# Kernel optimization log

Measured on AMD Instinct MI355X. Metric: run time of the kernel, lower is better.

The kernel has to match this reference:

```python
import jax, jax.numpy as jnp
import numpy as np

N, C, H, W = 64, 256, 56, 56
SIZE = 51          # odd number of spline knots per activation
GRID = 0.1         # knot spacing


def setup_inputs() -> dict:
    key = jax.random.key(0)
    x = jax.random.normal(key, (N, C, H, W), dtype=jnp.float32)

    # Coefficient init identical to the module: first half of channels use |grid|,
    # second half use softshrink(grid, lambd=0.5).
    half_knots = SIZE // 2
    grid_arange = jnp.arange(-half_knots, half_knots + 1, dtype=jnp.float32) * GRID  # [SIZE]
    grid_tensor = jnp.broadcast_to(grid_arange, (C, SIZE))                           # [C, SIZE]
    halfC = C // 2
    softshrunk = jnp.where(grid_tensor > 0.5, grid_tensor - 0.5,
                           jnp.where(grid_tensor < -0.5, grid_tensor + 0.5, 0.0))
    coeffs = jnp.concatenate([jnp.abs(grid_tensor[:halfC]), softshrunk[halfC:]], axis=0)
    coefficients_vect = coeffs.reshape(-1)                                           # [C*SIZE]

    zero_knot_indexes = jnp.arange(C, dtype=jnp.int32) * SIZE + half_knots           # [C]
    return {"x": x, "coefficients_vect": coefficients_vect,
            "zero_knot_indexes": zero_knot_indexes}


def reference(x, coefficients_vect, zero_knot_indexes):
    half_knots = SIZE // 2
    # Clamp so that idx and idx+1 stay inside this activation's knot range.
    x_clamped = jnp.clip(x, -GRID * half_knots, GRID * (half_knots - 1))
    floored = jnp.floor(x_clamped / GRID)               # left knot offset (float)
    fracs = x / GRID - floored                          # fractional position (uses unclamped x)
    idx = zero_knot_indexes[None, :, None, None] + floored.astype(jnp.int32)  # [N,C,H,W]
    c0 = coefficients_vect[idx]
    c1 = coefficients_vect[idx + 1]
    return c1 * fracs + c0 * (1.0 - fracs)
```

## Files before the change

### kernel.cpp

```cpp
#include <hip/hip_runtime.h>


typedef float f32x4 __attribute__((ext_vector_type(4)));

constexpr int C_CH  = 256;
constexpr int KSIZE = 51;
constexpr int HW    = 56 * 56;
constexpr int HW4   = HW / 4;

__device__ __forceinline__ f32x4 bspline4(f32x4 v, const float2* sc, int bias) {
    f32x4 r;
    #pragma unroll
    for (int k = 0; k < 4; ++k) {
        float xe = v[k];
        float xc = fminf(fmaxf(xe, -2.5f), 2.4f);
        float fl = floorf(xc * 10.0f);
        float fr = xe * 10.0f - fl;
        float2 cc = sc[(int)fl + bias];
        r[k] = cc.y * fr + cc.x * (1.0f - fr);
    }
    return r;
}

__global__ __launch_bounds__(256)
void bspline_act_kernel(const float* __restrict__ x,
                        const float* __restrict__ coeff,
                        const int*   __restrict__ zk,
                        float*       __restrict__ out)
{
    const int p   = blockIdx.x;
    const int c   = p & (C_CH - 1);
    const int tid = threadIdx.x;

    __shared__ float2 sc[KSIZE - 1];
    if (tid < KSIZE - 1) {
        float a = coeff[c * KSIZE + tid];
        float b = coeff[c * KSIZE + tid + 1];
        sc[tid] = make_float2(a, b);
    }
    const int bias = zk[c] - c * KSIZE;
    __syncthreads();

    const f32x4* __restrict__ xv = (const f32x4*)(x + (size_t)p * HW);
    f32x4*       __restrict__ ov = (f32x4*)(out + (size_t)p * HW);

    f32x4 v0 = __builtin_nontemporal_load(&xv[tid]);
    f32x4 v1 = __builtin_nontemporal_load(&xv[tid + 256]);
    f32x4 v2 = __builtin_nontemporal_load(&xv[tid + 512]);
    const bool tail = tid < (HW4 - 768);
    f32x4 v3;
    if (tail) v3 = __builtin_nontemporal_load(&xv[tid + 768]);

    f32x4 r0 = bspline4(v0, sc, bias);
    f32x4 r1 = bspline4(v1, sc, bias);
    f32x4 r2 = bspline4(v2, sc, bias);
    __builtin_nontemporal_store(r0, &ov[tid]);
    __builtin_nontemporal_store(r1, &ov[tid + 256]);
    __builtin_nontemporal_store(r2, &ov[tid + 512]);
    if (tail) {
        f32x4 r3 = bspline4(v3, sc, bias);
        __builtin_nontemporal_store(r3, &ov[tid + 768]);
    }
}

extern "C" void kernel_launch(void* const* d_in, const int* in_sizes, int n_in,
                              void* d_out, int out_size, void* d_ws, size_t ws_size,
                              hipStream_t stream) {
    const float* x     = (const float*)d_in[0];
    const float* coeff = (const float*)d_in[1];
    const int*   zk    = (const int*)d_in[2];
    float*       out   = (float*)d_out;

    const int n_planes = out_size / HW;
    bspline_act_kernel<<<n_planes, 256, 0, stream>>>(x, coeff, zk, out);
}
```

Measured before the change: 68.87 us.

## Process eight batch planes per block with register double-buffered loads

```diff
diff --git a/kernel.cpp b/kernel.cpp
--- a/kernel.cpp
+++ b/kernel.cpp
@@ -7,6 +7,7 @@
 constexpr int KSIZE = 51;
 constexpr int HW    = 56 * 56;
 constexpr int HW4   = HW / 4;
+constexpr int PPB   = 8;
 
 __device__ __forceinline__ f32x4 bspline4(f32x4 v, const float2* sc, int bias) {
     f32x4 r;
@@ -28,38 +29,53 @@
                         const int*   __restrict__ zk,
                         float*       __restrict__ out)
 {
-    const int p   = blockIdx.x;
-    const int c   = p & (C_CH - 1);
+    const int bid = blockIdx.x;
+    const int c   = bid & (C_CH - 1);
+    const int n0  = (bid >> 8) * PPB;
     const int tid = threadIdx.x;
+
+    const size_t  base    = ((size_t)n0 * C_CH + c) * HW;
+    const size_t  vstride = (size_t)C_CH * HW / 4;
+    const f32x4* __restrict__ xv = (const f32x4*)(x + base);
+    f32x4*       __restrict__ ov = (f32x4*)(out + base);
+
+    const bool tail = tid < (HW4 - 768);
+
+    f32x4 a0 = __builtin_nontemporal_load(xv + tid);
+    f32x4 a1 = __builtin_nontemporal_load(xv + tid + 256);
+    f32x4 a2 = __builtin_nontemporal_load(xv + tid + 512);
+    f32x4 a3 = {0,0,0,0};
+    if (tail) a3 = __builtin_nontemporal_load(xv + tid + 768);
 
     __shared__ float2 sc[KSIZE - 1];
     if (tid < KSIZE - 1) {
-        float a = coeff[c * KSIZE + tid];
-        float b = coeff[c * KSIZE + tid + 1];
-        sc[tid] = make_float2(a, b);
+        float va = coeff[c * KSIZE + tid];
+        float vb = coeff[c * KSIZE + tid + 1];
+        sc[tid] = make_float2(va, vb);
     }
     const int bias = zk[c] - c * KSIZE;
     __syncthreads();
 
-    const f32x4* __restrict__ xv = (const f32x4*)(x + (size_t)p * HW);
-    f32x4*       __restrict__ ov = (f32x4*)(out + (size_t)p * HW);
-
-    f32x4 v0 = __builtin_nontemporal_load(&xv[tid]);
-    f32x4 v1 = __builtin_nontemporal_load(&xv[tid + 256]);
-    f32x4 v2 = __builtin_nontemporal_load(&xv[tid + 512]);
-    const bool tail = tid < (HW4 - 768);
-    f32x4 v3;
-    if (tail) v3 = __builtin_nontemporal_load(&xv[tid + 768]);
-
-    f32x4 r0 = bspline4(v0, sc, bias);
-    f32x4 r1 = bspline4(v1, sc, bias);
-    f32x4 r2 = bspline4(v2, sc, bias);
-    __builtin_nontemporal_store(r0, &ov[tid]);
-    __builtin_nontemporal_store(r1, &ov[tid + 256]);
-    __builtin_nontemporal_store(r2, &ov[tid + 512]);
-    if (tail) {
-        f32x4 r3 = bspline4(v3, sc, bias);
-        __builtin_nontemporal_store(r3, &ov[tid + 768]);
+    #pragma unroll
+    for (int pl = 0; pl < PPB; ++pl) {
+        f32x4 b0, b1, b2, b3;
+        if (pl + 1 < PPB) {
+            const f32x4* xn = xv + (size_t)(pl + 1) * vstride;
+            b0 = __builtin_nontemporal_load(xn + tid);
+            b1 = __builtin_nontemporal_load(xn + tid + 256);
+            b2 = __builtin_nontemporal_load(xn + tid + 512);
+            if (tail) b3 = __builtin_nontemporal_load(xn + tid + 768);
+        }
+        f32x4* oc = ov + (size_t)pl * vstride;
+        __builtin_nontemporal_store(bspline4(a0, sc, bias), oc + tid);
+        __builtin_nontemporal_store(bspline4(a1, sc, bias), oc + tid + 256);
+        __builtin_nontemporal_store(bspline4(a2, sc, bias), oc + tid + 512);
+        if (tail)
+            __builtin_nontemporal_store(bspline4(a3, sc, bias), oc + tid + 768);
+        if (pl + 1 < PPB) {
+            a0 = b0; a1 = b1; a2 = b2;
+            if (tail) a3 = b3;
+        }
     }
 }
 
@@ -72,5 +88,6 @@
     float*       out   = (float*)d_out;
 
     const int n_planes = out_size / HW;
-    bspline_act_kernel<<<n_planes, 256, 0, stream>>>(x, coeff, zk, out);
+    const int blocks   = n_planes / PPB;
+    bspline_act_kernel<<<blocks, 256, 0, stream>>>(x, coeff, zk, out);
 }
```

After: 73.04 us. 6.1% more time.
